# Optimization experiments

Hardware: AMD Instinct MI355X
Metric: run time of the kernel (lower is better)

The kernel has to match this reference:

```python
import jax, jax.numpy as jnp
import numpy as np

V, C, D = 131072, 64, 8


def setup_inputs() -> dict:
    key = jax.random.key(0)
    kx, kw = jax.random.split(key)
    x = jax.random.normal(kx, (V, C * D), dtype=jnp.float32)
    # Stacked per-channel Linear weights: W[c] has torch layout (out, in) = (D, D).
    # (Original init is identity; random weights exercise the same math.)
    W = jax.random.normal(kw, (C, D, D), dtype=jnp.float32)
    return {"x": x, "W": W}


def reference(x, W):
    # x: (V, C*D) -> (V, D, C) as in torch reshape(x.shape[0], D, -1)
    c, d = W.shape[0], W.shape[1]
    xr = x.reshape(x.shape[0], d, c)
    # Ox[v, e, j] = sum_d xr[v, d, j] * W[j, e, d]   (torch Linear: y = x @ W.T)
    # einsum 'bki,bkj->bi' contracts k AND sums over j of Ox, so precompute
    # s[v, k] = sum_j Ox[v, k, j] in one fused contraction:
    s = jnp.einsum('vdc,ckd->vk', xr, W)          # (V, D)
    xOx = jnp.einsum('vk,vki->vi', s, xr)         # (V, C)
    return jnp.tanh(xOx)
```

## Files before the change

kernel.cpp:

```cpp
#include <hip/hip_runtime.h>
#include <hip/hip_bf16.h>


__device__ __forceinline__ float fast_tanh(float x) {
    float e = __expf(2.0f * x);
    return 1.0f - 2.0f / (e + 1.0f);
}

__device__ __forceinline__ float fold16(float a, float b, int lane) {
    float x   = (lane & 16) ? a : b;
    float sh  = __shfl_xor(x, 16, 64);
    float own = (lane & 16) ? b : a;
    return own + sh;
}

__device__ __forceinline__ float fold32(float a, float b, int lane) {
    float x   = (lane & 32) ? a : b;
    float sh  = __shfl_xor(x, 32, 64);
    float own = (lane & 32) ? b : a;
    return own + sh;
}

template <int CTRL>
__device__ __forceinline__ float dpp_add(float v) {
    int i = __builtin_bit_cast(int, v);
    int p = __builtin_amdgcn_update_dpp(i, i, CTRL, 0xF, 0xF, false);
    return v + __builtin_bit_cast(float, p);
}

__device__ __forceinline__ float row16_sum(float v) {
    v = dpp_add<0xB1>(v);
    v = dpp_add<0x4E>(v);
    v = dpp_add<0x141>(v);
    v = dpp_add<0x140>(v);
    return v;
}

__global__ __launch_bounds__(256, 4)
void ipf_kernel(const float* __restrict__ x, const float* __restrict__ W,
                float* __restrict__ out, int V) {
    const int tid  = blockIdx.x * blockDim.x + threadIdx.x;
    const int lane = threadIdx.x & 63;
    const int wave = tid >> 6;
    const int nwav = (gridDim.x * blockDim.x) >> 6;

    const int d0 = lane >> 4;
    const int c0 = (lane & 15) << 2;

    float Wa[4][8], Wb[4][8];
#pragma unroll
    for (int j = 0; j < 4; ++j) {
        const float* wp = W + (size_t)(c0 + j) * 64 + d0;
#pragma unroll
        for (int k = 0; k < 8; ++k) {
            Wa[j][k] = wp[k * 8];
            Wb[j][k] = wp[k * 8 + 4];
        }
    }

    const float4* __restrict__ x4 = reinterpret_cast<const float4*>(x);

    int v = wave;
    if (v >= V) return;
    float4 a = x4[(size_t)v * 128 + lane];
    float4 b = x4[(size_t)v * 128 + 64 + lane];

    while (true) {
        const int vn = v + nwav;
        const bool more = (vn < V);
        float4 an = a, bn = b;
        if (more) {
            an = x4[(size_t)vn * 128 + lane];
            bn = x4[(size_t)vn * 128 + 64 + lane];
        }

        const float xa[4] = {a.x, a.y, a.z, a.w};
        const float xb[4] = {b.x, b.y, b.z, b.w};

        float p[8];
#pragma unroll
        for (int k = 0; k < 8; ++k) {
            float acc = 0.0f;
#pragma unroll
            for (int j = 0; j < 4; ++j) {
                acc = fmaf(xa[j], Wa[j][k], acc);
                acc = fmaf(xb[j], Wb[j][k], acc);
            }
            p[k] = acc;
        }

#pragma unroll
        for (int k = 0; k < 8; ++k) p[k] = row16_sum(p[k]);

        float t0 = fold16(p[0], p[1], lane);
        float t1 = fold16(p[2], p[3], lane);
        float t2 = fold16(p[4], p[5], lane);
        float t3 = fold16(p[6], p[7], lane);
        float u = fold32(t0, t1, lane);
        float w = fold32(t2, t3, lane);

        float q0 = fmaf(u, xa[0], w * xb[0]);
        float q1 = fmaf(u, xa[1], w * xb[1]);
        float q2 = fmaf(u, xa[2], w * xb[2]);
        float q3 = fmaf(u, xa[3], w * xb[3]);

        float A = fold16(q0, q1, lane);
        float B = fold16(q2, q3, lane);
        float r = fold32(A, B, lane);

        const int col = ((lane & 15) << 2) + d0;
        out[(size_t)v * 64 + col] = fast_tanh(r);

        if (!more) break;
        v = vn; a = an; b = bn;
    }
}

extern "C" void kernel_launch(void* const* d_in, const int* in_sizes, int n_in,
                              void* d_out, int out_size, void* d_ws, size_t ws_size,
                              hipStream_t stream) {
    const float* x = (const float*)d_in[0];
    const float* W = (const float*)d_in[1];
    float* out = (float*)d_out;
    const int V = in_sizes[0] / 512;

    const int block = 256;
    const int grid  = 2048;
    ipf_kernel<<<grid, block, 0, stream>>>(x, W, out, V);
}
```

Measured before the change: 92.22 us.

## Process two rows per iteration with deeper prefetch and deferred row reduction

Each wave now handles two rows per loop iteration and prefetches both next rows, doubling the number of loads in flight. The per-k row16 DPP reductions are moved after the cross-lane folds, so only two row16 sums run instead of eight. Occupancy hint drops from 4 to 3 blocks per SIMD to leave room for the extra registers. The loop assumes V divides evenly by 2*nwav and clamps out-of-range prefetch indices to row 0, so any remainder rows would be skipped.

New measurement: 95.75 us. 1.04x slower.

```diff
diff --git a/kernel.cpp b/kernel.cpp
--- a/kernel.cpp
+++ b/kernel.cpp
@@ -1,6 +1,7 @@
 #include <hip/hip_runtime.h>
-#include <hip/hip_bf16.h>
 
+
+typedef float f32x4 __attribute__((ext_vector_type(4)));
 
 __device__ __forceinline__ float fast_tanh(float x) {
     float e = __expf(2.0f * x);
@@ -36,7 +37,7 @@
     return v;
 }
 
-__global__ __launch_bounds__(256, 4)
+__global__ __launch_bounds__(256, 3)
 void ipf_kernel(const float* __restrict__ x, const float* __restrict__ W,
                 float* __restrict__ out, int V) {
     const int tid  = blockIdx.x * blockDim.x + threadIdx.x;
@@ -58,22 +59,9 @@
         }
     }
 
-    const float4* __restrict__ x4 = reinterpret_cast<const float4*>(x);
+    const f32x4* __restrict__ x4 = reinterpret_cast<const f32x4*>(x);
 
-    int v = wave;
-    if (v >= V) return;
-    float4 a = x4[(size_t)v * 128 + lane];
-    float4 b = x4[(size_t)v * 128 + 64 + lane];
-
-    while (true) {
-        const int vn = v + nwav;
-        const bool more = (vn < V);
-        float4 an = a, bn = b;
-        if (more) {
-            an = x4[(size_t)vn * 128 + lane];
-            bn = x4[(size_t)vn * 128 + 64 + lane];
-        }
-
+    auto process_row = [&](const f32x4& a, const f32x4& b, int v) {
         const float xa[4] = {a.x, a.y, a.z, a.w};
         const float xb[4] = {b.x, b.y, b.z, b.w};
 
@@ -89,15 +77,14 @@
             p[k] = acc;
         }
 
-#pragma unroll
-        for (int k = 0; k < 8; ++k) p[k] = row16_sum(p[k]);
-
         float t0 = fold16(p[0], p[1], lane);
         float t1 = fold16(p[2], p[3], lane);
         float t2 = fold16(p[4], p[5], lane);
         float t3 = fold16(p[6], p[7], lane);
         float u = fold32(t0, t1, lane);
         float w = fold32(t2, t3, lane);
+        u = row16_sum(u);
+        w = row16_sum(w);
 
         float q0 = fmaf(u, xa[0], w * xb[0]);
         float q1 = fmaf(u, xa[1], w * xb[1]);
@@ -110,9 +97,31 @@
 
         const int col = ((lane & 15) << 2) + d0;
         out[(size_t)v * 64 + col] = fast_tanh(r);
+    };
 
-        if (!more) break;
-        v = vn; a = an; b = bn;
+    const int niter = V / (2 * nwav);
+    int vA = wave;
+    int vB = wave + nwav;
+    if (vA >= V) return;
+
+    f32x4 aA = x4[(size_t)vA * 128 + lane];
+    f32x4 bA = x4[(size_t)vA * 128 + 64 + lane];
+    f32x4 aB = x4[(size_t)vB * 128 + lane];
+    f32x4 bB = x4[(size_t)vB * 128 + 64 + lane];
+
+    for (int it = 0; it < niter; ++it) {
+        int vA2 = vA + 2 * nwav; vA2 = (vA2 < V) ? vA2 : 0;
+        int vB2 = vB + 2 * nwav; vB2 = (vB2 < V) ? vB2 : 0;
+        f32x4 aA2 = x4[(size_t)vA2 * 128 + lane];
+        f32x4 bA2 = x4[(size_t)vA2 * 128 + 64 + lane];
+        f32x4 aB2 = x4[(size_t)vB2 * 128 + lane];
+        f32x4 bB2 = x4[(size_t)vB2 * 128 + 64 + lane];
+
+        process_row(aA, bA, vA);
+        process_row(aB, bB, vB);
+
+        vA = vA2; vB = vB2;
+        aA = aA2; bA = bA2; aB = aB2; bB = bB2;
     }
 }
 
```
